# Kernel optimization log

Hardware: AMD Instinct MI355X
Metric: run time of the kernel (lower is better)

## Reference

```python
import jax, jax.numpy as jnp
import numpy as np
from jax import lax

SQRT_HALF = 0.7071067811865476
LAYERS = 20
STACKS = 2
LAYERS_PER_STACK = LAYERS // STACKS
K = 3
OUT_CH = 256
RES_CH = 64
GATE_CH = 128
SKIP_CH = 256
CIN_CH = 80


def setup_inputs() -> dict:
    key = jax.random.key(0)
    ks = jax.random.split(key, 20)
    s = 0.05
    inp = {
        'x': jax.random.normal(ks[0], (4, OUT_CH, 16384), jnp.float32),
        'c': jax.random.normal(ks[1], (4, CIN_CH, 16384), jnp.float32),
        # first conv: kernel size 2 (Conv1d2x1), out_channels -> residual_channels
        'W_first': jax.random.normal(ks[2], (RES_CH, OUT_CH, 2), jnp.float32) * s,
        'b_first': jnp.zeros((RES_CH,), jnp.float32),
        # per-layer dilated conv (residual -> gate), stacked over layers
        'W_dil': jax.random.normal(ks[3], (LAYERS, GATE_CH, RES_CH, K), jnp.float32) * s,
        'b_dil': jnp.zeros((LAYERS, GATE_CH), jnp.float32),
        # per-layer local-conditioning 1x1 (cin -> gate)
        'W_c': jax.random.normal(ks[4], (LAYERS, GATE_CH, CIN_CH), jnp.float32) * s,
        'b_c': jnp.zeros((LAYERS, GATE_CH), jnp.float32),
        # per-layer 1x1 skip (gate/2 -> skip) and out (gate/2 -> residual)
        'W_skip': jax.random.normal(ks[5], (LAYERS, SKIP_CH, GATE_CH // 2), jnp.float32) * s,
        'b_skip': jnp.zeros((LAYERS, SKIP_CH), jnp.float32),
        'W_out': jax.random.normal(ks[6], (LAYERS, RES_CH, GATE_CH // 2), jnp.float32) * s,
        'b_out': jnp.zeros((LAYERS, RES_CH), jnp.float32),
        # final 1x1 convs
        'W_last1': jax.random.normal(ks[7], (SKIP_CH, SKIP_CH), jnp.float32) * s,
        'b_last1': jnp.zeros((SKIP_CH,), jnp.float32),
        'W_last2': jax.random.normal(ks[8], (OUT_CH, SKIP_CH), jnp.float32) * s,
        'b_last2': jnp.zeros((OUT_CH,), jnp.float32),
    }
    return inp


def reference(x, c, W_first, b_first, W_dil, b_dil, W_c, b_c,
              W_skip, b_skip, W_out, b_out, W_last1, b_last1, W_last2, b_last2):
    dn = ('NCH', 'OIH', 'NCH')
    # first conv: F.pad(x, (1,0)) then kernel-2 conv == causal left pad 1
    h = lax.conv_general_dilated(x, W_first, (1,), [(1, 0)], dimension_numbers=dn)
    h = jnp.tanh(h + b_first[None, :, None])  # hparams.use_tanh_embed
    skips = None
    for l in range(LAYERS):
        d = 2 ** (l % LAYERS_PER_STACK)
        # causal dilated conv: pad left (K-1)*d
        y = lax.conv_general_dilated(h, W_dil[l], (1,), [((K - 1) * d, 0)],
                                     rhs_dilation=(d,), dimension_numbers=dn)
        y = y + b_dil[l][None, :, None]
        cond = jnp.einsum('bct,gc->bgt', c, W_c[l]) + b_c[l][None, :, None]
        a, b = jnp.split(y + cond, 2, axis=1)  # gated activation units
        z = jnp.tanh(a) * jax.nn.sigmoid(b)
        s = jnp.einsum('bgt,sg->bst', z, W_skip[l]) + b_skip[l][None, :, None]
        h = (jnp.einsum('bgt,rg->brt', z, W_out[l]) + b_out[l][None, :, None] + h) * SQRT_HALF
        if skips is None:
            skips = s
        else:
            skips = (skips + s) * SQRT_HALF  # faithful to original accumulation
    out = jax.nn.relu(skips)
    out = jnp.einsum('bst,os->bot', out, W_last1) + b_last1[None, :, None]
    out = jax.nn.relu(out)
    out = jnp.einsum('bst,os->bot', out, W_last2) + b_last2[None, :, None]
    return out
```

## Files before the change

### kernel.cpp

```cpp
#include <hip/hip_runtime.h>
#include <math.h>


#define T_LEN   16384
#define NB      4
#define BT      (NB * T_LEN)
#define NLAYERS 20
#define SQH     0.70710678118654752440f

typedef _Float16 half8 __attribute__((ext_vector_type(8)));
typedef _Float16 half4 __attribute__((ext_vector_type(4)));
typedef float f32x4 __attribute__((ext_vector_type(4)));

__device__ inline f32x4 mfma16(half8 a, half8 b, f32x4 c) {
  return __builtin_amdgcn_mfma_f32_16x16x32_f16(a, b, c, 0, 0, 0);
}

__global__ __launch_bounds__(256) void prep_pack(
    const float* __restrict__ Wf, const float* __restrict__ Wdil,
    const float* __restrict__ Wc, const float* __restrict__ Wskip,
    const float* __restrict__ Wout, const float* __restrict__ Wl1,
    const float* __restrict__ Wl2, const float* __restrict__ bdil,
    const float* __restrict__ bc, const float* __restrict__ bskip,
    _Float16* __restrict__ wdp, _Float16* __restrict__ wcp,
    _Float16* __restrict__ wop, _Float16* __restrict__ wskp,
    _Float16* __restrict__ wfp, _Float16* __restrict__ wl1p,
    _Float16* __restrict__ wl2p, float* __restrict__ bde,
    float* __restrict__ bsk)
{
  const float Q = 0.70710678118654752440f;
  const int WDP_E = 20 * 3 * 128 * 64;
  const int WCP_E = 20 * 128 * 96;
  const int WOP_E = 20 * 64 * 64;
  const int WSK_E = 256 * 1280;
  const int WFP_E = 64 * 512;
  const int WL_E  = 256 * 256;
  const int BDE_E = 20 * 128;
  const int BSK_E = 256;
  const int TOTAL = WDP_E + WCP_E + WOP_E + WSK_E + WFP_E + 2 * WL_E + BDE_E + BSK_E;
  for (int i = blockIdx.x * blockDim.x + threadIdx.x; i < TOTAL;
       i += gridDim.x * blockDim.x) {
    int j = i;
    if (j < WDP_E) {
      int l = j / (3 * 128 * 64); int r2 = j % (3 * 128 * 64);
      int tau = r2 / (128 * 64);  int r3 = r2 % (128 * 64);
      int n = r3 >> 6; int kc = r3 & 63;
      wdp[j] = (_Float16)Wdil[((l * 128 + n) * 64 + kc) * 3 + tau];
      continue;
    }
    j -= WDP_E;
    if (j < WCP_E) {
      int l = j / (128 * 96); int r2 = j % (128 * 96);
      int n = r2 / 96; int kc = r2 % 96;
      wcp[j] = (_Float16)(kc < 80 ? Wc[(l * 128 + n) * 80 + kc] : 0.f);
      continue;
    }
    j -= WCP_E;
    if (j < WOP_E) {
      int l = j >> 12; int r2 = j & 4095;
      int n = r2 >> 6; int kc = r2 & 63;
      wop[j] = (_Float16)Wout[(l * 64 + n) * 64 + kc];
      continue;
    }
    j -= WOP_E;
    if (j < WSK_E) {
      int n = j / 1280; int k = j % 1280;
      int l = k >> 6; int kc = k & 63;
      float f = (l == 0) ? 1.f : powf(Q, (float)(1 - l));
      wskp[j] = (_Float16)(Wskip[(l * 256 + n) * 64 + kc] * f);
      continue;
    }
    j -= WSK_E;
    if (j < WFP_E) {
      int n = j >> 9; int k = j & 511;
      int tau = k >> 8; int ci = k & 255;
      wfp[j] = (_Float16)Wf[(n * 256 + ci) * 2 + tau];
      continue;
    }
    j -= WFP_E;
    if (j < WL_E) { wl1p[j] = (_Float16)Wl1[j]; continue; }
    j -= WL_E;
    if (j < WL_E) { wl2p[j] = (_Float16)Wl2[j]; continue; }
    j -= WL_E;
    if (j < BDE_E) { bde[j] = bdil[j] + bc[j]; continue; }
    j -= BDE_E;
    {
      int n = j;
      float s = 0.f;
      for (int l = 0; l < NLAYERS; ++l) {
        float w = powf(Q, (float)(l == 0 ? 19 : 20 - l));
        s += bskip[l * 256 + n] * w;
      }
      bsk[n] = s;
    }
  }
}

__global__ __launch_bounds__(256) void tr_kernel(
    const float* __restrict__ src, _Float16* __restrict__ dst, int C, int Cpad, int CB)
{
  __shared__ float tile[32 * 33];
  int bid = blockIdx.x;
  int cb = bid % CB;
  int tb = (bid / CB) % (T_LEN / 32);
  int bb = bid / (CB * (T_LEN / 32));
  int t0 = tb * 32, ch0 = cb * 32;
  int tl = threadIdx.x & 31, cl = threadIdx.x >> 5;
#pragma unroll
  for (int i = 0; i < 4; ++i) {
    int ch = cl + 8 * i;
    float v = (ch0 + ch < C) ? src[((size_t)bb * C + ch0 + ch) * T_LEN + t0 + tl] : 0.f;
    tile[ch * 33 + tl] = v;
  }
  __syncthreads();
  int t = threadIdx.x >> 3;
  int c4 = (threadIdx.x & 7) * 4;
  half4 hv = {(_Float16)tile[(c4 + 0) * 33 + t], (_Float16)tile[(c4 + 1) * 33 + t],
              (_Float16)tile[(c4 + 2) * 33 + t], (_Float16)tile[(c4 + 3) * 33 + t]};
  *(half4*)&dst[((size_t)bb * T_LEN + t0 + t) * Cpad + ch0 + c4] = hv;
}

__global__ __launch_bounds__(256, 4) void first_conv(
    const _Float16* __restrict__ xt, const _Float16* __restrict__ wfp,
    const float* __restrict__ bf, _Float16* __restrict__ h0)
{
  __shared__ _Float16 As[128 * 72];
  __shared__ _Float16 Bs[64 * 72];
  const int tid = threadIdx.x;
  const int lane = tid & 63, w = tid >> 6;
  const int wx = w & 1, wy = w >> 1;
  const int l15 = lane & 15, quad = lane >> 4;
  const int p0 = blockIdx.x * 128;
  const int b = p0 >> 14, t0 = p0 & (T_LEN - 1);
  const int r = tid >> 1, halfo = (tid & 1) * 32;

  f32x4 acc[4][2];
#pragma unroll
  for (int mi = 0; mi < 4; ++mi)
#pragma unroll
    for (int ni = 0; ni < 2; ++ni) { f32x4 z = {0.f, 0.f, 0.f, 0.f}; acc[mi][ni] = z; }

  for (int s = 0; s < 8; ++s) {
    int tau = s >> 2, ci0 = (s & 3) * 64;
    int ts = t0 + r - 1 + tau;
    if (ts >= 0) {
      const uint4* src = (const uint4*)(xt + ((size_t)(b * T_LEN + ts) * 256 + ci0 + halfo));
#pragma unroll
      for (int j = 0; j < 4; ++j) *(uint4*)&As[r * 72 + halfo + 8 * j] = src[j];
    } else {
      uint4 z = {0, 0, 0, 0};
#pragma unroll
      for (int j = 0; j < 4; ++j) *(uint4*)&As[r * 72 + halfo + 8 * j] = z;
    }
    if (tid < 128) {
      const uint4* s4 = (const uint4*)(wfp + ((size_t)r * 512 + tau * 256 + ci0 + halfo));
#pragma unroll
      for (int j = 0; j < 4; ++j) *(uint4*)&Bs[r * 72 + halfo + 8 * j] = s4[j];
    }
    __syncthreads();
#pragma unroll
    for (int kc = 0; kc < 2; ++kc) {
      const int k0 = kc * 32 + quad * 8;
      half8 af[4], bfr[2];
#pragma unroll
      for (int mi = 0; mi < 4; ++mi)
        af[mi] = *(const half8*)&As[(64 * wy + 16 * mi + l15) * 72 + k0];
#pragma unroll
      for (int ni = 0; ni < 2; ++ni)
        bfr[ni] = *(const half8*)&Bs[(32 * wx + 16 * ni + l15) * 72 + k0];
#pragma unroll
      for (int mi = 0; mi < 4; ++mi)
#pragma unroll
        for (int ni = 0; ni < 2; ++ni)
          acc[mi][ni] = mfma16(af[mi], bfr[ni], acc[mi][ni]);
    }
    __syncthreads();
  }
#pragma unroll
  for (int mi = 0; mi < 4; ++mi)
#pragma unroll
    for (int ni = 0; ni < 2; ++ni) {
      int col = 32 * wx + 16 * ni + l15;
      int rowb = 64 * wy + 16 * mi + quad * 4;
      float bo = bf[col];
      size_t base = ((size_t)p0 + rowb) * 64 + col;
#pragma unroll
      for (int reg = 0; reg < 4; ++reg) {
        float v = acc[mi][ni][reg] + bo;
        float e = __expf(2.f * v);
        h0[base + (size_t)64 * reg] = (_Float16)(1.f - 2.f * __builtin_amdgcn_rcpf(e + 1.f));
      }
    }
}

__global__ __launch_bounds__(512, 4) void layer_kernel(
    const _Float16* __restrict__ hprev, _Float16* __restrict__ hnext,
    const _Float16* __restrict__ ctp,
    const _Float16* __restrict__ wdp_l, const _Float16* __restrict__ wcp_l,
    const _Float16* __restrict__ wop_l,
    const float* __restrict__ bde_l, const float* __restrict__ bout_l,
    _Float16* __restrict__ zslot, int d, int last)
{
  __shared__ _Float16 A0[128 * 72];
  __shared__ _Float16 A1[128 * 72];
  __shared__ _Float16 B0[128 * 72];
  __shared__ _Float16 B1[128 * 72];
  __shared__ float bde_s[128];

  const int tid = threadIdx.x;
  const int lane = tid & 63, w = tid >> 6;
  const int wx = w & 1, wy = w >> 1;
  const int l15 = lane & 15, quad = lane >> 4;
  const int p0 = blockIdx.x * 128;
  const int b = p0 >> 14, t0 = p0 & (T_LEN - 1);
  const int r2 = tid >> 2, qo = (tid & 3) * 16;
  const int o8 = (tid & 3) * 8;

  if (tid < 128) bde_s[tid] = bde_l[tid];

  f32x4 acc[2][4];
#pragma unroll
  for (int mi = 0; mi < 2; ++mi)
#pragma unroll
    for (int ni = 0; ni < 4; ++ni) { f32x4 z = {0.f, 0.f, 0.f, 0.f}; acc[mi][ni] = z; }

  uint4 pa0, pa1, pb0, pb1;
  bool paz = false;

  auto issue = [&](int s) {
    if (s >= 2) {
      int ts = t0 + r2 - (4 - s) * d;
      paz = (ts < 0);
      int tsc = paz ? 0 : ts;
      const uint4* src = (const uint4*)(hprev + ((size_t)(b * T_LEN + tsc) * 64 + qo));
      pa0 = src[0]; pa1 = src[1];
      const uint4* sb = (const uint4*)(wdp_l + ((size_t)(s - 2) * 8192 + r2 * 64 + qo));
      pb0 = sb[0]; pb1 = sb[1];
    } else if (s == 0) {
      paz = false;
      const uint4* sa = (const uint4*)(ctp + ((size_t)(p0 + r2) * 96 + qo));
      pa0 = sa[0]; pa1 = sa[1];
      const uint4* sb = (const uint4*)(wcp_l + ((size_t)r2 * 96 + qo));
      pb0 = sb[0]; pb1 = sb[1];
    } else {
      paz = false;
      pa0 = *(const uint4*)(ctp + ((size_t)(p0 + r2) * 96 + 64 + o8));
      pb0 = *(const uint4*)(wcp_l + ((size_t)r2 * 96 + 64 + o8));
    }
  };
  auto commit = [&](int s) {
    _Float16* A = (s & 1) ? A1 : A0;
    _Float16* B = (s & 1) ? B1 : B0;
    if (s == 1) {
      *(uint4*)&A[r2 * 72 + o8] = pa0;
      *(uint4*)&B[r2 * 72 + o8] = pb0;
    } else {
      if (!paz) {
        *(uint4*)&A[r2 * 72 + qo] = pa0;
        *(uint4*)&A[r2 * 72 + qo + 8] = pa1;
      } else {
        uint4 z4 = {0, 0, 0, 0};
        *(uint4*)&A[r2 * 72 + qo] = z4;
        *(uint4*)&A[r2 * 72 + qo + 8] = z4;
      }
      *(uint4*)&B[r2 * 72 + qo] = pb0;
      *(uint4*)&B[r2 * 72 + qo + 8] = pb1;
    }
  };

  issue(0);
  commit(0);
#pragma unroll 1
  for (int s = 0; s < 5; ++s) {
    if (s < 4) issue(s + 1);
    __syncthreads();
    const _Float16* A = (s & 1) ? A1 : A0;
    const _Float16* B = (s & 1) ? B1 : B0;
    const int nkc = (s == 1) ? 1 : 2;
    for (int kc = 0; kc < nkc; ++kc) {
      const int k0 = kc * 32 + quad * 8;
      half8 af[2], bfr[4];
#pragma unroll
      for (int mi = 0; mi < 2; ++mi)
        af[mi] = *(const half8*)&A[(32 * wy + 16 * mi + l15) * 72 + k0];
#pragma unroll
      for (int ni = 0; ni < 4; ++ni) {
        int ncol = 32 * wx + 16 * (ni & 1) + 64 * (ni >> 1);
        bfr[ni] = *(const half8*)&B[(ncol + l15) * 72 + k0];
      }
#pragma unroll
      for (int mi = 0; mi < 2; ++mi)
#pragma unroll
        for (int ni = 0; ni < 4; ++ni)
          acc[mi][ni] = mfma16(af[mi], bfr[ni], acc[mi][ni]);
    }
    if (s < 4) commit(s + 1);
  }

#pragma unroll
  for (int mi = 0; mi < 2; ++mi)
#pragma unroll
    for (int ni2 = 0; ni2 < 2; ++ni2) {
      int colb = 32 * wx + 16 * ni2 + l15;
      float ba = bde_s[colb], bb = bde_s[colb + 64];
#pragma unroll
      for (int reg = 0; reg < 4; ++reg) {
        float av = acc[mi][ni2][reg] + ba;
        float gv = acc[mi][ni2 + 2][reg] + bb;
        float ea = __expf(2.f * av);
        float th = 1.f - 2.f * __builtin_amdgcn_rcpf(ea + 1.f);
        float sg = __builtin_amdgcn_rcpf(1.f + __expf(-gv));
        A1[(32 * wy + 16 * mi + quad * 4 + reg) * 72 + colb] = (_Float16)(th * sg);
      }
    }

  if (!last && tid < 256) {
    int row = tid >> 2;
    const uint4* sb = (const uint4*)(wop_l + ((size_t)row * 64 + qo));
    *(uint4*)&B1[row * 72 + qo] = sb[0];
    *(uint4*)&B1[row * 72 + qo + 8] = sb[1];
  }
  __syncthreads();

  {
    uint4 v0 = *(const uint4*)&A1[r2 * 72 + qo];
    uint4 v1 = *(const uint4*)&A1[r2 * 72 + qo + 8];
    uint4* dst = (uint4*)(zslot + ((size_t)(p0 + r2) * 64 + qo));
    dst[0] = v0; dst[1] = v1;
  }

  if (last) return;

  f32x4 a4[2][2];
#pragma unroll
  for (int mi = 0; mi < 2; ++mi)
#pragma unroll
    for (int ni = 0; ni < 2; ++ni) { f32x4 z = {0.f, 0.f, 0.f, 0.f}; a4[mi][ni] = z; }
#pragma unroll
  for (int kc = 0; kc < 2; ++kc) {
    const int k0 = kc * 32 + quad * 8;
    half8 af[2], bfr[2];
#pragma unroll
    for (int mi = 0; mi < 2; ++mi)
      af[mi] = *(const half8*)&A1[(32 * wy + 16 * mi + l15) * 72 + k0];
#pragma unroll
    for (int ni = 0; ni < 2; ++ni)
      bfr[ni] = *(const half8*)&B1[(32 * wx + 16 * ni + l15) * 72 + k0];
#pragma unroll
    for (int mi = 0; mi < 2; ++mi)
#pragma unroll
      for (int ni = 0; ni < 2; ++ni)
        a4[mi][ni] = mfma16(af[mi], bfr[ni], a4[mi][ni]);
  }
#pragma unroll
  for (int mi = 0; mi < 2; ++mi)
#pragma unroll
    for (int ni = 0; ni < 2; ++ni) {
      int col = 32 * wx + 16 * ni + l15;
      int rowb = 32 * wy + 16 * mi + quad * 4;
      float bo = bout_l[col];
#pragma unroll
      for (int reg = 0; reg < 4; ++reg) {
        float hv = (float)A0[(rowb + reg) * 72 + col];
        A0[(rowb + reg) * 72 + col] = (_Float16)((a4[mi][ni][reg] + bo + hv) * SQH);
      }
    }
  __syncthreads();
  {
    uint4 v0 = *(const uint4*)&A0[r2 * 72 + qo];
    uint4 v1 = *(const uint4*)&A0[r2 * 72 + qo + 8];
    uint4* dst = (uint4*)(hnext + ((size_t)(p0 + r2) * 64 + qo));
    dst[0] = v0; dst[1] = v1;
  }
}

__global__ __launch_bounds__(512, 4) void flush_kernel(
    const _Float16* __restrict__ zbuf, const _Float16* __restrict__ wskp,
    _Float16* __restrict__ Abuf, const float* __restrict__ bsk,
    _Float16* __restrict__ skr, int l0, int g, int mode)
{
  __shared__ _Float16 As[128 * 72];
  __shared__ _Float16 Bs0[128 * 72];
  __shared__ _Float16 Bs1[128 * 72];
  const int tid = threadIdx.x;
  const int half = tid >> 8;
  _Float16* Bsh = half ? Bs1 : Bs0;
  const int tloc = tid & 255;
  const int lane = tloc & 63, w4 = tloc >> 6;
  const int wx = w4 & 1, wy = w4 >> 1;
  const int l15 = lane & 15, quad = lane >> 4;
  const int p0 = blockIdx.x * 128;
  const int n0 = half * 128;
  const int r = tloc >> 1, halfo = (tloc & 1) * 32;

  f32x4 acc[4][4];
#pragma unroll
  for (int mi = 0; mi < 4; ++mi)
#pragma unroll
    for (int ni = 0; ni < 4; ++ni) { f32x4 z = {0.f, 0.f, 0.f, 0.f}; acc[mi][ni] = z; }

#pragma unroll 1
  for (int j = 0; j < g; ++j) {
    const int lj = l0 + j;
    const _Float16* zsl = zbuf + (size_t)(lj & 7) * ((size_t)BT * 64);
    if (half == 0) {
      const uint4* sa = (const uint4*)(zsl + ((size_t)(p0 + r) * 64 + halfo));
#pragma unroll
      for (int jj = 0; jj < 4; ++jj) *(uint4*)&As[r * 72 + halfo + 8 * jj] = sa[jj];
    }
    const uint4* sb = (const uint4*)(wskp + ((size_t)(n0 + r) * 1280 + lj * 64 + halfo));
#pragma unroll
    for (int jj = 0; jj < 4; ++jj) *(uint4*)&Bsh[r * 72 + halfo + 8 * jj] = sb[jj];
    __syncthreads();
#pragma unroll
    for (int kc = 0; kc < 2; ++kc) {
      const int k0 = kc * 32 + quad * 8;
      half8 af[4], bfr[4];
#pragma unroll
      for (int mi = 0; mi < 4; ++mi)
        af[mi] = *(const half8*)&As[(64 * wy + 16 * mi + l15) * 72 + k0];
#pragma unroll
      for (int ni = 0; ni < 4; ++ni)
        bfr[ni] = *(const half8*)&Bsh[(64 * wx + 16 * ni + l15) * 72 + k0];
#pragma unroll
      for (int mi = 0; mi < 4; ++mi)
#pragma unroll
        for (int ni = 0; ni < 4; ++ni)
          acc[mi][ni] = mfma16(af[mi], bfr[ni], acc[mi][ni]);
    }
    __syncthreads();
  }
  const float Q19 = 0.0013810679320049757f;
#pragma unroll
  for (int mi = 0; mi < 4; ++mi)
#pragma unroll
    for (int ni = 0; ni < 4; ++ni) {
      int col = n0 + 64 * wx + 16 * ni + l15;
      int rowb = 64 * wy + 16 * mi + quad * 4;
      size_t base = ((size_t)p0 + rowb) * 256 + col;
      if (mode == 2) {
        float bb = bsk[col];
#pragma unroll
        for (int reg = 0; reg < 4; ++reg) {
          float v = (acc[mi][ni][reg] + (float)Abuf[base + (size_t)256 * reg]) * Q19 + bb;
          skr[base + (size_t)256 * reg] = (_Float16)(v > 0.f ? v : 0.f);
        }
      } else if (mode == 1) {
#pragma unroll
        for (int reg = 0; reg < 4; ++reg) {
          size_t a = base + (size_t)256 * reg;
          Abuf[a] = (_Float16)((float)Abuf[a] + acc[mi][ni][reg]);
        }
      } else {
#pragma unroll
        for (int reg = 0; reg < 4; ++reg)
          Abuf[base + (size_t)256 * reg] = (_Float16)acc[mi][ni][reg];
      }
    }
}

__global__ __launch_bounds__(256, 4) void gemm256(
    const _Float16* __restrict__ Asrc, const _Float16* __restrict__ Bp,
    const float* __restrict__ bias, void* __restrict__ dst, int mode)
{
  __shared__ _Float16 smem[2 * 128 * 72];
  _Float16* As = smem;
  _Float16* Bs = smem + 128 * 72;
  const int tid = threadIdx.x;
  const int lane = tid & 63, w = tid >> 6;
  const int wx = w & 1, wy = w >> 1;
  const int l15 = lane & 15, quad = lane >> 4;
  const int p0 = blockIdx.x * 128;
  const int n0 = blockIdx.y * 128;
  const int r = tid >> 1, halfo = (tid & 1) * 32;

  f32x4 acc[4][4];
#pragma unroll
  for (int mi = 0; mi < 4; ++mi)
#pragma unroll
    for (int ni = 0; ni < 4; ++ni) { f32x4 z = {0.f, 0.f, 0.f, 0.f}; acc[mi][ni] = z; }

  for (int c4 = 0; c4 < 4; ++c4) {
    int k0g = c4 * 64;
    const uint4* sa = (const uint4*)(Asrc + ((size_t)(p0 + r) * 256 + k0g + halfo));
#pragma unroll
    for (int jj = 0; jj < 4; ++jj) *(uint4*)&As[r * 72 + halfo + 8 * jj] = sa[jj];
    const uint4* sb = (const uint4*)(Bp + ((size_t)(n0 + r) * 256 + k0g + halfo));
#pragma unroll
    for (int jj = 0; jj < 4; ++jj) *(uint4*)&Bs[r * 72 + halfo + 8 * jj] = sb[jj];
    __syncthreads();
#pragma unroll
    for (int kc = 0; kc < 2; ++kc) {
      const int k0 = kc * 32 + quad * 8;
      half8 af[4], bfr[4];
#pragma unroll
      for (int mi = 0; mi < 4; ++mi)
        af[mi] = *(const half8*)&As[(64 * wy + 16 * mi + l15) * 72 + k0];
#pragma unroll
      for (int ni = 0; ni < 4; ++ni)
        bfr[ni] = *(const half8*)&Bs[(64 * wx + 16 * ni + l15) * 72 + k0];
#pragma unroll
      for (int mi = 0; mi < 4; ++mi)
#pragma unroll
        for (int ni = 0; ni < 4; ++ni)
          acc[mi][ni] = mfma16(af[mi], bfr[ni], acc[mi][ni]);
    }
    __syncthreads();
  }
  if (mode == 0) {
#pragma unroll
    for (int mi = 0; mi < 4; ++mi)
#pragma unroll
      for (int ni = 0; ni < 4; ++ni) {
        int col = n0 + 64 * wx + 16 * ni + l15;
        int rowb = 64 * wy + 16 * mi + quad * 4;
        float bv = bias[col];
        _Float16* o = (_Float16*)dst;
#pragma unroll
        for (int reg = 0; reg < 4; ++reg) {
          float v = acc[mi][ni][reg] + bv;
          o[((size_t)(p0 + rowb + reg)) * 256 + col] = (_Float16)(v > 0.f ? v : 0.f);
        }
      }
  } else {
    float* Ts = (float*)smem;
    const int b = p0 >> 14, t0g = p0 & (T_LEN - 1);
    for (int pass = 0; pass < 2; ++pass) {
      if (wx == pass) {
#pragma unroll
        for (int mi = 0; mi < 4; ++mi)
#pragma unroll
          for (int ni = 0; ni < 4; ++ni) {
            int col_l = 16 * ni + l15;
            float bv = bias[n0 + 64 * pass + col_l];
            int tl = 64 * wy + 16 * mi + quad * 4;
#pragma unroll
            for (int reg = 0; reg < 4; ++reg)
              Ts[col_l * 132 + tl + reg] = acc[mi][ni][reg] + bv;
          }
      }
      __syncthreads();
      {
        int col_l = tid >> 2;
        int tq = (tid & 3) * 32;
        float* o = (float*)dst + ((size_t)b * 256 + n0 + 64 * pass + col_l) * T_LEN + t0g + tq;
#pragma unroll
        for (int j = 0; j < 8; ++j)
          *(float4*)(o + 4 * j) = *(const float4*)&Ts[col_l * 132 + tq + 4 * j];
      }
      __syncthreads();
    }
  }
}

extern "C" void kernel_launch(void* const* d_in, const int* in_sizes, int n_in,
                              void* d_out, int out_size, void* d_ws, size_t ws_size,
                              hipStream_t stream)
{
  const float* x     = (const float*)d_in[0];
  const float* c     = (const float*)d_in[1];
  const float* Wf    = (const float*)d_in[2];
  const float* bf    = (const float*)d_in[3];
  const float* Wdil  = (const float*)d_in[4];
  const float* bdil  = (const float*)d_in[5];
  const float* Wc    = (const float*)d_in[6];
  const float* bc    = (const float*)d_in[7];
  const float* Wskip = (const float*)d_in[8];
  const float* bskip = (const float*)d_in[9];
  const float* Wout  = (const float*)d_in[10];
  const float* bout  = (const float*)d_in[11];
  const float* Wl1   = (const float*)d_in[12];
  const float* bl1   = (const float*)d_in[13];
  const float* Wl2   = (const float*)d_in[14];
  const float* bl2   = (const float*)d_in[15];

  char* base = (char*)d_ws;
  _Float16* zbuf = (_Float16*)base;
  _Float16* xt   = zbuf;
  _Float16* skr  = zbuf + (size_t)4 * BT * 64;
  _Float16* y1   = zbuf;
  _Float16* ctp  = (_Float16*)(base + 67108864);
  _Float16* hA   = (_Float16*)(base + 79691776);
  _Float16* hB   = (_Float16*)(base + 88080384);
  _Float16* wdp  = (_Float16*)(base + 96468992);
  _Float16* wcp  = wdp  + (size_t)20 * 3 * 128 * 64;
  _Float16* wop  = wcp  + (size_t)20 * 128 * 96;
  _Float16* wskp = wop  + (size_t)20 * 64 * 64;
  _Float16* wfp  = wskp + (size_t)256 * 1280;
  _Float16* wl1p = wfp  + (size_t)64 * 512;
  _Float16* wl2p = wl1p + (size_t)256 * 256;
  float*    bde  = (float*)(wl2p + (size_t)256 * 256);
  float*    bsk  = bde + 20 * 128;
  _Float16* Abuf = (_Float16*)d_out;

  prep_pack<<<2048, 256, 0, stream>>>(Wf, Wdil, Wc, Wskip, Wout, Wl1, Wl2,
                                      bdil, bc, bskip,
                                      wdp, wcp, wop, wskp, wfp, wl1p, wl2p,
                                      bde, bsk);
  tr_kernel<<<NB * (T_LEN / 32) * 8, 256, 0, stream>>>(x, xt, 256, 256, 8);
  tr_kernel<<<NB * (T_LEN / 32) * 3, 256, 0, stream>>>(c, ctp, 80, 96, 3);
  first_conv<<<512, 256, 0, stream>>>(xt, wfp, bf, hA);

  const _Float16* hin = hA;
  _Float16* hout = hB;
  for (int l = 0; l < NLAYERS; ++l) {
    int d = 1 << (l % 10);
    layer_kernel<<<512, 512, 0, stream>>>(
        hin, hout, ctp,
        wdp + (size_t)l * 3 * 128 * 64, wcp + (size_t)l * 128 * 96,
        wop + (size_t)l * 64 * 64, bde + l * 128, bout + l * 64,
        zbuf + (size_t)(l & 7) * BT * 64, d, (l == NLAYERS - 1) ? 1 : 0);
    _Float16* tmp = (_Float16*)hin; hin = hout; hout = tmp;
    if (l == 7)  flush_kernel<<<512, 512, 0, stream>>>(zbuf, wskp, Abuf, bsk, skr, 0, 8, 0);
    if (l == 15) flush_kernel<<<512, 512, 0, stream>>>(zbuf, wskp, Abuf, bsk, skr, 8, 8, 1);
    if (l == 19) flush_kernel<<<512, 512, 0, stream>>>(zbuf, wskp, Abuf, bsk, skr, 16, 4, 2);
  }
  gemm256<<<dim3(512, 2), 256, 0, stream>>>(skr, wl1p, bl1, (void*)y1, 0);
  gemm256<<<dim3(512, 2), 256, 0, stream>>>(y1, wl2p, bl2, d_out, 1);
}
```

Before: 720.9 us.

## Swizzle block indices across XCDs and widen the x transpose tiles

Adds an XCD-aware block-index swizzle so that consecutive logical tiles land on the same XCD (blocks are dispatched round-robin over 8 XCDs). The swizzle is applied to the transpose, first-conv, layer, flush and final GEMM kernels. The x transpose gets its own kernel that moves 32x128 tiles with float4 loads and half8 stores, replacing the 32x32 scalar tile version. The aim is better L2 locality for the halo reads in the dilated convolutions and fewer, wider memory transactions in the transpose. The swizzle assumes the grid size is divisible by 8.

```diff
diff --git a/kernel.cpp b/kernel.cpp
--- a/kernel.cpp
+++ b/kernel.cpp
@@ -14,6 +14,10 @@
 
 __device__ inline f32x4 mfma16(half8 a, half8 b, f32x4 c) {
   return __builtin_amdgcn_mfma_f32_16x16x32_f16(a, b, c, 0, 0, 0);
+}
+
+__device__ __forceinline__ int xswz(int pb, int nwg) {
+  return (pb & 7) * (nwg >> 3) + (pb >> 3);
 }
 
 __global__ __launch_bounds__(256) void prep_pack(
@@ -96,14 +100,45 @@
   }
 }
 
+__global__ __launch_bounds__(256) void tr_x_kernel(
+    const float* __restrict__ src, _Float16* __restrict__ dst)
+{
+  __shared__ float tile[32 * 132];
+  const int lb = xswz(blockIdx.x, 4096);
+  const int row_tile = lb >> 3, cb = lb & 7;
+  const int bb = row_tile >> 7;
+  const int t0 = (row_tile & 127) * 128;
+  const int ch0 = cb * 32;
+  {
+    int ch = threadIdx.x >> 3, tq = (threadIdx.x & 7) * 16;
+    const float4* s4 = (const float4*)(src + ((size_t)(bb * 256 + ch0 + ch)) * T_LEN + t0 + tq);
+#pragma unroll
+    for (int j = 0; j < 4; ++j)
+      *(float4*)&tile[ch * 132 + tq + 4 * j] = s4[j];
+  }
+  __syncthreads();
+  {
+    int t = threadIdx.x >> 1, c16 = (threadIdx.x & 1) * 16;
+    half8 h0, h1;
+#pragma unroll
+    for (int j = 0; j < 8; ++j) {
+      h0[j] = (_Float16)tile[(c16 + j) * 132 + t];
+      h1[j] = (_Float16)tile[(c16 + 8 + j) * 132 + t];
+    }
+    _Float16* o = dst + ((size_t)(bb * T_LEN + t0 + t)) * 256 + ch0 + c16;
+    *(half8*)o = h0;
+    *(half8*)(o + 8) = h1;
+  }
+}
+
 __global__ __launch_bounds__(256) void tr_kernel(
     const float* __restrict__ src, _Float16* __restrict__ dst, int C, int Cpad, int CB)
 {
   __shared__ float tile[32 * 33];
-  int bid = blockIdx.x;
-  int cb = bid % CB;
-  int tb = (bid / CB) % (T_LEN / 32);
-  int bb = bid / (CB * (T_LEN / 32));
+  int lb = xswz(blockIdx.x, gridDim.x);
+  int cb = lb % CB;
+  int tb = (lb / CB) % (T_LEN / 32);
+  int bb = lb / (CB * (T_LEN / 32));
   int t0 = tb * 32, ch0 = cb * 32;
   int tl = threadIdx.x & 31, cl = threadIdx.x >> 5;
 #pragma unroll
@@ -130,7 +165,7 @@
   const int lane = tid & 63, w = tid >> 6;
   const int wx = w & 1, wy = w >> 1;
   const int l15 = lane & 15, quad = lane >> 4;
-  const int p0 = blockIdx.x * 128;
+  const int p0 = xswz(blockIdx.x, 512) * 128;
   const int b = p0 >> 14, t0 = p0 & (T_LEN - 1);
   const int r = tid >> 1, halfo = (tid & 1) * 32;
 
@@ -211,7 +246,7 @@
   const int lane = tid & 63, w = tid >> 6;
   const int wx = w & 1, wy = w >> 1;
   const int l15 = lane & 15, quad = lane >> 4;
-  const int p0 = blockIdx.x * 128;
+  const int p0 = xswz(blockIdx.x, 512) * 128;
   const int b = p0 >> 14, t0 = p0 & (T_LEN - 1);
   const int r2 = tid >> 2, qo = (tid & 3) * 16;
   const int o8 = (tid & 3) * 8;
@@ -389,7 +424,7 @@
   const int lane = tloc & 63, w4 = tloc >> 6;
   const int wx = w4 & 1, wy = w4 >> 1;
   const int l15 = lane & 15, quad = lane >> 4;
-  const int p0 = blockIdx.x * 128;
+  const int p0 = xswz(blockIdx.x, 512) * 128;
   const int n0 = half * 128;
   const int r = tloc >> 1, halfo = (tloc & 1) * 32;
 
@@ -470,7 +505,7 @@
   const int lane = tid & 63, w = tid >> 6;
   const int wx = w & 1, wy = w >> 1;
   const int l15 = lane & 15, quad = lane >> 4;
-  const int p0 = blockIdx.x * 128;
+  const int p0 = xswz(blockIdx.x, 512) * 128;
   const int n0 = blockIdx.y * 128;
   const int r = tid >> 1, halfo = (tid & 1) * 32;
 
@@ -597,7 +632,7 @@
                                       bdil, bc, bskip,
                                       wdp, wcp, wop, wskp, wfp, wl1p, wl2p,
                                       bde, bsk);
-  tr_kernel<<<NB * (T_LEN / 32) * 8, 256, 0, stream>>>(x, xt, 256, 256, 8);
+  tr_x_kernel<<<4096, 256, 0, stream>>>(x, xt);
   tr_kernel<<<NB * (T_LEN / 32) * 3, 256, 0, stream>>>(c, ctp, 80, 96, 3);
   first_conv<<<512, 256, 0, stream>>>(xt, wfp, bf, hA);
 
```

Result: no change. 711.6 us (-1.3%).
